# Kernel optimization log

Measured on AMD Instinct MI355X. Metric: run time of the kernel, lower is better.

## Reference

```python
import jax, jax.numpy as jnp
import numpy as np
import math

D_MODEL = 512
DK = D_MODEL // 4      # per-head dim = 128
DH = D_MODEL // 8      # half-head dim = 64
BS, QL, SL = 4, 2048, 2048


def setup_inputs() -> dict:
    key = jax.random.key(0)
    ks = jax.random.split(key, 16)
    h = D_MODEL // 2
    inp = {
        "q": jax.random.normal(ks[0], (2, BS, QL, h), jnp.float32),
        "k": jax.random.normal(ks[1], (2, BS, SL, h), jnp.float32),
        "v": jax.random.normal(ks[2], (2, BS, SL, h), jnp.float32),
        "q_spa_embed": jax.random.normal(ks[3], (BS, 1, DK, DK), jnp.float32) * 0.1,
        "kv_spa_embed": jax.random.normal(ks[4], (BS, SL, DK, DK), jnp.float32) * 0.1,
        "attention_bias": jax.random.normal(ks[5], (BS, SL), jnp.float32),
        "mask": jax.random.randint(ks[6], (BS, SL), 0, 2, jnp.int32),
        # Linear weights stored [in, out] (torch Linear(in,out).weight.T)
        "W_qa": jax.random.normal(ks[7], (h, h // 2), jnp.float32) / math.sqrt(h),
        "W_qb": jax.random.normal(ks[8], (h, h // 2), jnp.float32) / math.sqrt(h),
        "W_ka": jax.random.normal(ks[9], (h, h // 2), jnp.float32) / math.sqrt(h),
        "W_kb": jax.random.normal(ks[10], (h, h // 2), jnp.float32) / math.sqrt(h),
        "W_va": jax.random.normal(ks[11], (h, h // 2), jnp.float32) / math.sqrt(h),
        "W_vb": jax.random.normal(ks[12], (h, h // 2), jnp.float32) / math.sqrt(h),
        "W_oa": jax.random.normal(ks[13], (h, h), jnp.float32) / math.sqrt(h),
        "W_ob": jax.random.normal(ks[14], (h, h), jnp.float32) / math.sqrt(h),
    }
    return inp


def _make_heads(xa, xb):
    # xa, xb: [bs, L, d_model//4] -> [bs, 4, L, dk] with head pattern
    # (a0,b0),(a1,b0),(a0,b1),(a1,b1)
    bs, L, _ = xa.shape
    xa = xa.reshape(bs, L, 2, DH)
    xb = xb.reshape(bs, L, 2, DH)
    xa = jnp.tile(xa, (1, 1, 2, 1))            # [bs,L,4,DH]
    xb = jnp.repeat(xb, 2, axis=2)             # [bs,L,4,DH]
    return jnp.concatenate([xa, xb], axis=-1).transpose(0, 2, 1, 3)  # [bs,4,L,DK]


def reference(q, k, v, q_spa_embed, kv_spa_embed, attention_bias, mask,
              W_qa, W_qb, W_ka, W_kb, W_va, W_vb, W_oa, W_ob):
    bs, ql = q.shape[1], q.shape[2]
    sl = k.shape[2]
    qh = _make_heads(q[0] @ W_qa, q[1] @ W_qb)   # [bs,4,ql,DK]
    kh = _make_heads(k[0] @ W_ka, k[1] @ W_kb)   # [bs,4,sl,DK]
    vh = _make_heads(v[0] @ W_va, v[1] @ W_vb)   # [bs,4,sl,DK]

    # per-token spatial rotation (seq_len == kv_spa_embed.shape[1] branch)
    qh = jnp.einsum('bij,bhqj->bhqi', q_spa_embed[:, 0], qh)
    kh = jnp.einsum('bsij,bhsj->bhsi', kv_spa_embed, kh)

    scores = jnp.einsum('bhqd,bhsd->bhqs', qh, kh) / math.sqrt(D_MODEL // 4)
    scores = scores + mask.astype(scores.dtype)[:, None, None, :] * (-1e9)
    attn = jax.nn.softmax(scores - attention_bias[:, None, None, :], axis=-1)
    # dropout: identity (eval mode)
    out = jnp.einsum('bhqs,bhsd->bhqd', attn, vh)          # [bs,4,ql,DK]

    out = out.reshape(bs, 4, ql, 2, DH)
    oa = out[:, :, :, 0].transpose(0, 2, 1, 3).reshape(bs, ql, -1) @ W_oa
    ob = out[:, :, :, 1].transpose(0, 2, 1, 3).reshape(bs, ql, -1) @ W_ob
    return jnp.stack([oa, ob], axis=0), attn
```

## Files before the change

kernel.cpp:

```cpp
#include <hip/hip_runtime.h>
#include <math.h>

#define QL 2048
#define SL 2048
#define BS 4
#define NH 4
#define FSZ ((size_t)BS * QL * 128)

typedef short bf16x8 __attribute__((ext_vector_type(8)));
typedef float f32x4 __attribute__((ext_vector_type(4)));

__device__ __forceinline__ short to_bf16_rne(float x) {
    unsigned u = __float_as_uint(x);
    unsigned r = u + 0x7fffu + ((u >> 16) & 1u);
    return (short)(r >> 16);
}

__global__ __launch_bounds__(256) void proj_gemm(
    const float* __restrict__ q, const float* __restrict__ k, const float* __restrict__ v,
    const float* __restrict__ Wqa, const float* __restrict__ Wqb,
    const float* __restrict__ Wka, const float* __restrict__ Wkb,
    const float* __restrict__ Wva, const float* __restrict__ Wvb,
    float* __restrict__ ws)
{
    int id = blockIdx.z;
    const float* X; const float* W;
    const size_t HALF = (size_t)BS * QL * 256;
    switch (id) {
      case 0: X = q;        W = Wqa; break;
      case 1: X = q + HALF; W = Wqb; break;
      case 2: X = k;        W = Wka; break;
      case 3: X = k + HALF; W = Wkb; break;
      case 4: X = v;        W = Wva; break;
      default:X = v + HALF; W = Wvb; break;
    }
    float* Y = ws + (size_t)id * FSZ;
    int m0 = blockIdx.x * 64;
    int n0 = blockIdx.y * 64;
    __shared__ float At[64][68];
    __shared__ float Bt[64][68];
    int t = threadIdx.x;
    int tx = t & 15, ty = t >> 4;
    float acc[4][4] = {};
    for (int kc = 0; kc < 256; kc += 64) {
        for (int f = t; f < 1024; f += 256) {
            int row = f >> 4, c4 = (f & 15) * 4;
            *(float4*)&At[row][c4] = *(const float4*)(X + (size_t)(m0 + row) * 256 + kc + c4);
        }
        for (int f = t; f < 1024; f += 256) {
            int row = f >> 4, c4 = (f & 15) * 4;
            *(float4*)&Bt[row][c4] = *(const float4*)(W + (size_t)(kc + row) * 128 + n0 + c4);
        }
        __syncthreads();
        for (int j = 0; j < 64; j += 4) {
            float4 a4[4], b4[4];
            #pragma unroll
            for (int i = 0; i < 4; i++) a4[i] = *(const float4*)&At[ty * 4 + i][j];
            #pragma unroll
            for (int jj = 0; jj < 4; jj++) b4[jj] = *(const float4*)&Bt[j + jj][tx * 4];
            #pragma unroll
            for (int i = 0; i < 4; i++) {
                #pragma unroll
                for (int jj = 0; jj < 4; jj++) {
                    float av = ((const float*)&a4[i])[jj];
                    acc[i][0] += av * b4[jj].x;
                    acc[i][1] += av * b4[jj].y;
                    acc[i][2] += av * b4[jj].z;
                    acc[i][3] += av * b4[jj].w;
                }
            }
        }
        __syncthreads();
    }
    for (int i = 0; i < 4; i++) {
        float4 o = make_float4(acc[i][0], acc[i][1], acc[i][2], acc[i][3]);
        *(float4*)(Y + (size_t)(m0 + ty * 4 + i) * 128 + n0 + tx * 4) = o;
    }
}

__global__ __launch_bounds__(256) void rot_kernel(
    const float* __restrict__ ha, const float* __restrict__ hb,
    const float* __restrict__ E0, int per_token,
    float* __restrict__ outp)
{
    int tkn = blockIdx.x;
    int b = blockIdx.y;
    const float* E = E0 + (per_token ? ((size_t)(b * SL + tkn) * 16384)
                                     : ((size_t)b * 16384));
    __shared__ float hv[4][128];
    __shared__ float outl[4][128];
    int tid = threadIdx.x;
    size_t tok = (size_t)(b * QL + tkn) * 128;
    for (int idx = tid; idx < 512; idx += 256) {
        int h = idx >> 7, d = idx & 127;
        float val = (d < 64) ? ha[tok + (h & 1) * 64 + d]
                             : hb[tok + (h >> 1) * 64 + (d - 64)];
        hv[h][d] = val;
    }
    __syncthreads();
    int w = tid >> 6, lane = tid & 63;
    int half = lane >> 5, l5 = lane & 31;
    for (int it = 0; it < 16; ++it) {
        int i = w * 32 + it * 2 + half;
        float4 e = *(const float4*)(E + (size_t)i * 128 + l5 * 4);
        float acc[4];
        #pragma unroll
        for (int h = 0; h < 4; h++) {
            float4 x = *(const float4*)&hv[h][l5 * 4];
            acc[h] = e.x * x.x + e.y * x.y + e.z * x.z + e.w * x.w;
        }
        #pragma unroll
        for (int off = 1; off < 32; off <<= 1) {
            #pragma unroll
            for (int h = 0; h < 4; h++) acc[h] += __shfl_xor(acc[h], off);
        }
        if (l5 < 4) outl[l5][i] = acc[l5];
    }
    __syncthreads();
    for (int idx = tid; idx < 512; idx += 256) {
        int h = idx >> 7, d = idx & 127;
        outp[((size_t)(b * NH + h) * QL + tkn) * 128 + d] = outl[h][d];
    }
}

__global__ __launch_bounds__(256) void score_mfma_kernel(
    const float* __restrict__ qrot, const float* __restrict__ krot,
    const float* __restrict__ bias, const int* __restrict__ mask,
    float* __restrict__ attn, float* __restrict__ stats)
{
    __shared__ short lA[128 * 64];
    __shared__ short lB[128 * 64];
    __shared__ float redM[128][2];
    __shared__ float redS[128][2];

    int bid = blockIdx.x;
    int wg = (bid & 7) * 512 + (bid >> 3);
    int bh = wg >> 8;
    int qt = (wg >> 4) & 15, st = wg & 15;
    int q0 = qt * 128, s0 = st * 128;
    int b = bh >> 2;

    const float* Ag = qrot + ((size_t)bh * QL + q0) * 128;
    const float* Bg = krot + ((size_t)bh * SL + s0) * 128;

    int t = threadIdx.x;
    int srow = t >> 1, shalf = t & 1;
    int l = t & 63, w = t >> 6;
    int wr = w >> 1, wc = w & 1;
    int lr = l & 15, kb = l >> 4;

    f32x4 acc[4][4] = {};

    for (int kc = 0; kc < 128; kc += 32) {
        {
            const float* srcA = Ag + (size_t)srow * 128 + kc + shalf * 16;
            const float* srcB = Bg + (size_t)srow * 128 + kc + shalf * 16;
            float xa[16], xb[16];
            #pragma unroll
            for (int j = 0; j < 4; j++) {
                *(float4*)&xa[j * 4] = *(const float4*)(srcA + j * 4);
                *(float4*)&xb[j * 4] = *(const float4*)(srcB + j * 4);
            }
            bf16x8 aH0, aL0, aH1, aL1, bH0, bL0, bH1, bL1;
            #pragma unroll
            for (int j = 0; j < 8; j++) {
                short h = to_bf16_rne(xa[j]);
                float hf = __uint_as_float(((unsigned)(unsigned short)h) << 16);
                aH0[j] = h; aL0[j] = to_bf16_rne(xa[j] - hf);
                h = to_bf16_rne(xa[j + 8]);
                hf = __uint_as_float(((unsigned)(unsigned short)h) << 16);
                aH1[j] = h; aL1[j] = to_bf16_rne(xa[j + 8] - hf);
                h = to_bf16_rne(xb[j]);
                hf = __uint_as_float(((unsigned)(unsigned short)h) << 16);
                bH0[j] = h; bL0[j] = to_bf16_rne(xb[j] - hf);
                h = to_bf16_rne(xb[j + 8]);
                hf = __uint_as_float(((unsigned)(unsigned short)h) << 16);
                bH1[j] = h; bL1[j] = to_bf16_rne(xb[j + 8] - hf);
            }
            int base = srow * 64, r7 = srow & 7;
            *(bf16x8*)&lA[base + (((4 * shalf + 0) ^ r7) * 8)] = aH0;
            *(bf16x8*)&lA[base + (((4 * shalf + 1) ^ r7) * 8)] = aL0;
            *(bf16x8*)&lA[base + (((4 * shalf + 2) ^ r7) * 8)] = aH1;
            *(bf16x8*)&lA[base + (((4 * shalf + 3) ^ r7) * 8)] = aL1;
            *(bf16x8*)&lB[base + (((4 * shalf + 0) ^ r7) * 8)] = bH0;
            *(bf16x8*)&lB[base + (((4 * shalf + 1) ^ r7) * 8)] = bL0;
            *(bf16x8*)&lB[base + (((4 * shalf + 2) ^ r7) * 8)] = bH1;
            *(bf16x8*)&lB[base + (((4 * shalf + 3) ^ r7) * 8)] = bL1;
        }
        __syncthreads();

        bf16x8 ah[4], al[4], bhv[4], blv[4];
        #pragma unroll
        for (int m = 0; m < 4; m++) {
            int r = wr * 64 + m * 16 + lr;
            int r7 = r & 7, base = r * 64;
            ah[m] = *(bf16x8*)&lA[base + (((2 * kb + 0) ^ r7) * 8)];
            al[m] = *(bf16x8*)&lA[base + (((2 * kb + 1) ^ r7) * 8)];
        }
        #pragma unroll
        for (int n = 0; n < 4; n++) {
            int r = wc * 64 + n * 16 + lr;
            int r7 = r & 7, base = r * 64;
            bhv[n] = *(bf16x8*)&lB[base + (((2 * kb + 0) ^ r7) * 8)];
            blv[n] = *(bf16x8*)&lB[base + (((2 * kb + 1) ^ r7) * 8)];
        }
        #pragma unroll
        for (int m = 0; m < 4; m++) {
            #pragma unroll
            for (int n = 0; n < 4; n++) {
                acc[m][n] = __builtin_amdgcn_mfma_f32_16x16x32_bf16(ah[m], bhv[n], acc[m][n], 0, 0, 0);
                acc[m][n] = __builtin_amdgcn_mfma_f32_16x16x32_bf16(ah[m], blv[n], acc[m][n], 0, 0, 0);
                acc[m][n] = __builtin_amdgcn_mfma_f32_16x16x32_bf16(al[m], bhv[n], acc[m][n], 0, 0, 0);
            }
        }
        __syncthreads();
    }

    const float scale = 0.08838834764831845f;
    #pragma unroll
    for (int n = 0; n < 4; n++) {
        int gs = s0 + wc * 64 + n * 16 + lr;
        float adj = -1e9f * (float)mask[b * SL + gs] - bias[b * SL + gs];
        #pragma unroll
        for (int m = 0; m < 4; m++) {
            int gq = q0 + wr * 64 + m * 16 + kb * 4;
            float* dst = attn + ((size_t)bh * QL + gq) * SL + gs;
            f32x4 c = acc[m][n];
            c[0] = c[0] * scale + adj;
            c[1] = c[1] * scale + adj;
            c[2] = c[2] * scale + adj;
            c[3] = c[3] * scale + adj;
            acc[m][n] = c;
            dst[0 * SL] = c[0];
            dst[1 * SL] = c[1];
            dst[2 * SL] = c[2];
            dst[3 * SL] = c[3];
        }
    }

    #pragma unroll
    for (int m = 0; m < 4; m++) {
        #pragma unroll
        for (int i = 0; i < 4; i++) {
            float rm = fmaxf(fmaxf(acc[m][0][i], acc[m][1][i]),
                             fmaxf(acc[m][2][i], acc[m][3][i]));
            rm = fmaxf(rm, __shfl_xor(rm, 1));
            rm = fmaxf(rm, __shfl_xor(rm, 2));
            rm = fmaxf(rm, __shfl_xor(rm, 4));
            rm = fmaxf(rm, __shfl_xor(rm, 8));
            if (lr == 0) redM[wr * 64 + m * 16 + kb * 4 + i][wc] = rm;
        }
    }
    __syncthreads();
    #pragma unroll
    for (int m = 0; m < 4; m++) {
        #pragma unroll
        for (int i = 0; i < 4; i++) {
            int row = wr * 64 + m * 16 + kb * 4 + i;
            float mt = fmaxf(redM[row][0], redM[row][1]);
            float es = __expf(acc[m][0][i] - mt) + __expf(acc[m][1][i] - mt)
                     + __expf(acc[m][2][i] - mt) + __expf(acc[m][3][i] - mt);
            es += __shfl_xor(es, 1);
            es += __shfl_xor(es, 2);
            es += __shfl_xor(es, 4);
            es += __shfl_xor(es, 8);
            if (lr == 0) redS[row][wc] = es;
        }
    }
    __syncthreads();
    if (t < 128) {
        float mt = fmaxf(redM[t][0], redM[t][1]);
        float es = redS[t][0] + redS[t][1];
        size_t r = (size_t)bh * QL + q0 + t;
        stats[(r * 16 + st) * 2 + 0] = mt;
        stats[(r * 16 + st) * 2 + 1] = es;
    }
}

__global__ __launch_bounds__(256) void sreduce_kernel(
    const float* __restrict__ stats,
    float* __restrict__ rowm, float* __restrict__ rowinv)
{
    int r = blockIdx.x * 256 + threadIdx.x;
    const float* src = stats + (size_t)r * 32;
    float4 p[8];
    #pragma unroll
    for (int j = 0; j < 8; j++) p[j] = *(const float4*)(src + j * 4);
    float m = -INFINITY;
    #pragma unroll
    for (int j = 0; j < 8; j++) { m = fmaxf(m, p[j].x); m = fmaxf(m, p[j].z); }
    float s = 0.f;
    #pragma unroll
    for (int j = 0; j < 8; j++) {
        s += p[j].y * __expf(p[j].x - m);
        s += p[j].w * __expf(p[j].z - m);
    }
    rowm[r] = m;
    rowinv[r] = 1.0f / s;
}

__global__ __launch_bounds__(256) void vtrans_kernel(
    const float* __restrict__ va, const float* __restrict__ vb,
    short* __restrict__ vT)
{
    int sblk = blockIdx.x;
    int bh = blockIdx.y;
    int b = bh >> 2, h = bh & 3;
    int hao = (h & 1) * 64, hbo = (h >> 1) * 64;
    __shared__ float vt[32][132];
    int t = threadIdx.x;
    for (int f = t; f < 1024; f += 256) {
        int s = f >> 5, c4 = (f & 31) * 4;
        size_t tok = (size_t)(b * SL + sblk * 32 + s) * 128;
        float4 vv = (c4 < 64) ? *(const float4*)(va + tok + hao + c4)
                              : *(const float4*)(vb + tok + hbo + (c4 - 64));
        *(float4*)&vt[s][c4] = vv;
    }
    __syncthreads();
    int d = t >> 1, shalf = t & 1;
    bf16x8 hi[2], lo[2];
    #pragma unroll
    for (int kb2 = 0; kb2 < 2; kb2++) {
        int kb = shalf * 2 + kb2;
        #pragma unroll
        for (int j = 0; j < 8; j++) {
            float x = vt[kb * 8 + j][d];
            short hh = to_bf16_rne(x);
            float hf = __uint_as_float(((unsigned)(unsigned short)hh) << 16);
            hi[kb2][j] = hh;
            lo[kb2][j] = to_bf16_rne(x - hf);
        }
    }
    size_t base = (((size_t)bh * 64 + sblk) * 128 + d) * 64;
    int d7 = d & 7;
    *(bf16x8*)&vT[base + (size_t)(((2 * (shalf * 2 + 0) + 0) ^ d7) * 8)] = hi[0];
    *(bf16x8*)&vT[base + (size_t)(((2 * (shalf * 2 + 0) + 1) ^ d7) * 8)] = lo[0];
    *(bf16x8*)&vT[base + (size_t)(((2 * (shalf * 2 + 1) + 0) ^ d7) * 8)] = hi[1];
    *(bf16x8*)&vT[base + (size_t)(((2 * (shalf * 2 + 1) + 1) ^ d7) * 8)] = lo[1];
}

__global__ __launch_bounds__(256) void pv_fused_kernel(
    float* __restrict__ attn, const short* __restrict__ vT,
    const float* __restrict__ rowm, const float* __restrict__ rowinv,
    float* __restrict__ outh)
{
    __shared__ short lA[128 * 64];
    __shared__ short lB[128 * 64];

    int bid = blockIdx.x;
    int wg = (bid & 7) * 32 + (bid >> 3);
    int bh = wg >> 4, qt = wg & 15;
    int q0 = qt * 128;

    float* Ag = attn + ((size_t)bh * QL + q0) * SL;
    const short* Bg = vT + (size_t)bh * 64 * 8192;

    int t = threadIdx.x;
    int srow = t >> 1, shalf = t & 1;
    int l = t & 63, w = t >> 6;
    int wr = w >> 1, wc = w & 1;
    int lr = l & 15, kb = l >> 4;

    float rm  = rowm[(size_t)bh * QL + q0 + srow];
    float riv = rowinv[(size_t)bh * QL + q0 + srow];

    f32x4 acc[4][4] = {};

    for (int sblk = 0; sblk < 64; sblk++) {
        {
            float* src = Ag + (size_t)srow * SL + sblk * 32 + shalf * 16;
            float x[16];
            #pragma unroll
            for (int j = 0; j < 4; j++)
                *(float4*)&x[j * 4] = *(const float4*)(src + j * 4);
            #pragma unroll
            for (int j = 0; j < 16; j++)
                x[j] = __expf(x[j] - rm) * riv;
            #pragma unroll
            for (int j = 0; j < 4; j++)
                *(float4*)(src + j * 4) = *(float4*)&x[j * 4];
            bf16x8 h0, l0, h1, l1;
            #pragma unroll
            for (int j = 0; j < 8; j++) {
                short hh = to_bf16_rne(x[j]);
                float hf = __uint_as_float(((unsigned)(unsigned short)hh) << 16);
                h0[j] = hh; l0[j] = to_bf16_rne(x[j] - hf);
                hh = to_bf16_rne(x[j + 8]);
                hf = __uint_as_float(((unsigned)(unsigned short)hh) << 16);
                h1[j] = hh; l1[j] = to_bf16_rne(x[j + 8] - hf);
            }
            int base = srow * 64, r7 = srow & 7;
            *(bf16x8*)&lA[base + (((4 * shalf + 0) ^ r7) * 8)] = h0;
            *(bf16x8*)&lA[base + (((4 * shalf + 1) ^ r7) * 8)] = l0;
            *(bf16x8*)&lA[base + (((4 * shalf + 2) ^ r7) * 8)] = h1;
            *(bf16x8*)&lA[base + (((4 * shalf + 3) ^ r7) * 8)] = l1;
        }
        {
            const bf16x8* src = (const bf16x8*)(Bg + (size_t)sblk * 8192) + t * 4;
            bf16x8 v0 = src[0], v1 = src[1], v2 = src[2], v3 = src[3];
            bf16x8* dst = (bf16x8*)lB + t * 4;
            dst[0] = v0; dst[1] = v1; dst[2] = v2; dst[3] = v3;
        }
        __syncthreads();

        bf16x8 ah[4], al[4], bhv[4], blv[4];
        #pragma unroll
        for (int m = 0; m < 4; m++) {
            int r = wr * 64 + m * 16 + lr;
            int r7 = r & 7, base = r * 64;
            ah[m] = *(bf16x8*)&lA[base + (((2 * kb + 0) ^ r7) * 8)];
            al[m] = *(bf16x8*)&lA[base + (((2 * kb + 1) ^ r7) * 8)];
        }
        #pragma unroll
        for (int n = 0; n < 4; n++) {
            int r = wc * 64 + n * 16 + lr;
            int r7 = r & 7, base = r * 64;
            bhv[n] = *(bf16x8*)&lB[base + (((2 * kb + 0) ^ r7) * 8)];
            blv[n] = *(bf16x8*)&lB[base + (((2 * kb + 1) ^ r7) * 8)];
        }
        #pragma unroll
        for (int m = 0; m < 4; m++) {
            #pragma unroll
            for (int n = 0; n < 4; n++) {
                acc[m][n] = __builtin_amdgcn_mfma_f32_16x16x32_bf16(ah[m], bhv[n], acc[m][n], 0, 0, 0);
                acc[m][n] = __builtin_amdgcn_mfma_f32_16x16x32_bf16(ah[m], blv[n], acc[m][n], 0, 0, 0);
                acc[m][n] = __builtin_amdgcn_mfma_f32_16x16x32_bf16(al[m], bhv[n], acc[m][n], 0, 0, 0);
            }
        }
        __syncthreads();
    }

    #pragma unroll
    for (int n = 0; n < 4; n++) {
        int gd = wc * 64 + n * 16 + lr;
        #pragma unroll
        for (int m = 0; m < 4; m++) {
            int gq = q0 + wr * 64 + m * 16 + kb * 4;
            float* dst = outh + ((size_t)bh * QL + gq) * 128 + gd;
            f32x4 c = acc[m][n];
            dst[0 * 128] = c[0];
            dst[1 * 128] = c[1];
            dst[2 * 128] = c[2];
            dst[3 * 128] = c[3];
        }
    }
}

__global__ __launch_bounds__(256) void oproj_kernel(
    const float* __restrict__ outh, const float* __restrict__ Woa, const float* __restrict__ Wob,
    float* __restrict__ outp)
{
    int bid = blockIdx.x;
    int sel = bid >> 9;
    int rem = bid & 511;
    int b = rem >> 7;
    int rem2 = rem & 127;
    int tt = rem2 >> 2, ot = rem2 & 3;
    int t0 = tt * 64, o0 = ot * 64;
    const float* W = sel ? Wob : Woa;
    int doff = sel ? 64 : 0;
    __shared__ float At[64][68];
    __shared__ float Bt[64][68];
    int t = threadIdx.x;
    int tx = t & 15, ty = t >> 4;
    float acc[4][4] = {};
    for (int kc = 0; kc < 256; kc += 64) {
        int h = kc >> 6;
        for (int f = t; f < 1024; f += 256) {
            int row = f >> 4, c4 = (f & 15) * 4;
            *(float4*)&At[row][c4] =
                *(const float4*)(outh + ((size_t)(b * NH + h) * QL + t0 + row) * 128 + doff + c4);
        }
        for (int f = t; f < 1024; f += 256) {
            int row = f >> 4, c4 = (f & 15) * 4;
            *(float4*)&Bt[row][c4] = *(const float4*)(W + (size_t)(kc + row) * 256 + o0 + c4);
        }
        __syncthreads();
        for (int j = 0; j < 64; j += 4) {
            float4 a4[4], b4[4];
            #pragma unroll
            for (int i = 0; i < 4; i++) a4[i] = *(const float4*)&At[ty * 4 + i][j];
            #pragma unroll
            for (int jj = 0; jj < 4; jj++) b4[jj] = *(const float4*)&Bt[j + jj][tx * 4];
            #pragma unroll
            for (int i = 0; i < 4; i++) {
                #pragma unroll
                for (int jj = 0; jj < 4; jj++) {
                    float av = ((const float*)&a4[i])[jj];
                    acc[i][0] += av * b4[jj].x;
                    acc[i][1] += av * b4[jj].y;
                    acc[i][2] += av * b4[jj].z;
                    acc[i][3] += av * b4[jj].w;
                }
            }
        }
        __syncthreads();
    }
    for (int i = 0; i < 4; i++) {
        float4 o = make_float4(acc[i][0], acc[i][1], acc[i][2], acc[i][3]);
        *(float4*)(outp + ((size_t)((sel * BS + b) * QL) + t0 + ty * 4 + i) * 256 + o0 + tx * 4) = o;
    }
}

extern "C" void kernel_launch(void* const* d_in, const int* in_sizes, int n_in,
                              void* d_out, int out_size, void* d_ws, size_t ws_size,
                              hipStream_t stream)
{
    const float* q    = (const float*)d_in[0];
    const float* k    = (const float*)d_in[1];
    const float* v    = (const float*)d_in[2];
    const float* qse  = (const float*)d_in[3];
    const float* kvse = (const float*)d_in[4];
    const float* bias = (const float*)d_in[5];
    const int*   mask = (const int*)d_in[6];
    const float* Wqa  = (const float*)d_in[7];
    const float* Wqb  = (const float*)d_in[8];
    const float* Wka  = (const float*)d_in[9];
    const float* Wkb  = (const float*)d_in[10];
    const float* Wva  = (const float*)d_in[11];
    const float* Wvb  = (const float*)d_in[12];
    const float* Woa  = (const float*)d_in[13];
    const float* Wob  = (const float*)d_in[14];

    float* outp = (float*)d_out;
    float* attn = outp + (size_t)2 * BS * QL * 256;

    float* ws     = (float*)d_ws;
    float* qa     = ws + 0 * FSZ;
    float* qb     = ws + 1 * FSZ;
    float* ka     = ws + 2 * FSZ;
    float* kb     = ws + 3 * FSZ;
    float* va     = ws + 4 * FSZ;
    float* vb     = ws + 5 * FSZ;
    float* qrot   = ws + 6 * FSZ;
    float* krot   = ws + 10 * FSZ;
    float* outh   = ws + 14 * FSZ;
    float* stats  = outh;
    short* vT     = (short*)(ws + 18 * FSZ);
    float* rowm   = ws + 22 * FSZ;
    float* rowinv = ws + 22 * FSZ + 32768;

    proj_gemm<<<dim3(128, 2, 6), 256, 0, stream>>>(q, k, v, Wqa, Wqb, Wka, Wkb, Wva, Wvb, ws);
    vtrans_kernel<<<dim3(64, 16), 256, 0, stream>>>(va, vb, vT);
    rot_kernel<<<dim3(QL, BS), 256, 0, stream>>>(qa, qb, qse, 0, qrot);
    rot_kernel<<<dim3(SL, BS), 256, 0, stream>>>(ka, kb, kvse, 1, krot);
    score_mfma_kernel<<<4096, 256, 0, stream>>>(qrot, krot, bias, mask, attn, stats);
    sreduce_kernel<<<128, 256, 0, stream>>>(stats, rowm, rowinv);
    pv_fused_kernel<<<256, 256, 0, stream>>>(attn, vT, rowm, rowinv, outh);
    oproj_kernel<<<1024, 256, 0, stream>>>(outh, Woa, Wob, outp);
}
```

Measured before the change: 687.7 us.

## Pre-split rotated Q/K into swizzled bf16 hi/lo tiles in rotation kernel

The rotation kernel now converts its output into bf16 hi/lo pairs and writes them in the exact swizzled LDS tile layout used by the score kernel. The score kernel then stages tiles with plain vector copies instead of loading fp32 and converting each tile. Q/K conversion is no longer repeated across the 16 tiles that reuse each Q or K block, and global bytes read per tile stay the same. In exchange the rotation kernel does extra conversion work, and only half its threads do the store.

```diff
diff --git a/kernel.cpp b/kernel.cpp
--- a/kernel.cpp
+++ b/kernel.cpp
@@ -78,10 +78,10 @@
     }
 }
 
-__global__ __launch_bounds__(256) void rot_kernel(
+__global__ __launch_bounds__(256) void rot_split_kernel(
     const float* __restrict__ ha, const float* __restrict__ hb,
     const float* __restrict__ E0, int per_token,
-    float* __restrict__ outp)
+    short* __restrict__ rotS)
 {
     int tkn = blockIdx.x;
     int b = blockIdx.y;
@@ -117,14 +117,35 @@
         if (l5 < 4) outl[l5][i] = acc[l5];
     }
     __syncthreads();
-    for (int idx = tid; idx < 512; idx += 256) {
-        int h = idx >> 7, d = idx & 127;
-        outp[((size_t)(b * NH + h) * QL + tkn) * 128 + d] = outl[h][d];
+    if (tid < 128) {
+        int h    = tid >> 5;
+        int kcid = (tid >> 3) & 3;
+        int s    = tid & 7;
+        int shalf = s >> 2;
+        int isLo  = s & 1;
+        int jbase = ((s >> 1) & 1) * 8;
+        int dbase = kcid * 32 + shalf * 16 + jbase;
+        bf16x8 outv;
+        #pragma unroll
+        for (int j = 0; j < 8; j++) {
+            float x = outl[h][dbase + j];
+            short hh = to_bf16_rne(x);
+            if (isLo) {
+                float hf = __uint_as_float(((unsigned)(unsigned short)hh) << 16);
+                outv[j] = to_bf16_rne(x - hf);
+            } else {
+                outv[j] = hh;
+            }
+        }
+        int bh = b * NH + h;
+        int row = tkn & 127;
+        size_t base = ((((size_t)bh * 16 + (tkn >> 7)) * 4 + kcid) * 128 + row) * 64;
+        *(bf16x8*)&rotS[base + (size_t)((s ^ (row & 7)) * 8)] = outv;
     }
 }
 
 __global__ __launch_bounds__(256) void score_mfma_kernel(
-    const float* __restrict__ qrot, const float* __restrict__ krot,
+    const short* __restrict__ qrotS, const short* __restrict__ krotS,
     const float* __restrict__ bias, const int* __restrict__ mask,
     float* __restrict__ attn, float* __restrict__ stats)
 {
@@ -140,52 +161,26 @@
     int q0 = qt * 128, s0 = st * 128;
     int b = bh >> 2;
 
-    const float* Ag = qrot + ((size_t)bh * QL + q0) * 128;
-    const float* Bg = krot + ((size_t)bh * SL + s0) * 128;
-
     int t = threadIdx.x;
-    int srow = t >> 1, shalf = t & 1;
     int l = t & 63, w = t >> 6;
     int wr = w >> 1, wc = w & 1;
     int lr = l & 15, kb = l >> 4;
 
+    const short* Abase = qrotS + (((size_t)bh * 16 + qt) * 4) * 8192;
+    const short* Bbase = krotS + (((size_t)bh * 16 + st) * 4) * 8192;
+
     f32x4 acc[4][4] = {};
 
-    for (int kc = 0; kc < 128; kc += 32) {
+    for (int kcid = 0; kcid < 4; kcid++) {
         {
-            const float* srcA = Ag + (size_t)srow * 128 + kc + shalf * 16;
-            const float* srcB = Bg + (size_t)srow * 128 + kc + shalf * 16;
-            float xa[16], xb[16];
-            #pragma unroll
-            for (int j = 0; j < 4; j++) {
-                *(float4*)&xa[j * 4] = *(const float4*)(srcA + j * 4);
-                *(float4*)&xb[j * 4] = *(const float4*)(srcB + j * 4);
-            }
-            bf16x8 aH0, aL0, aH1, aL1, bH0, bL0, bH1, bL1;
-            #pragma unroll
-            for (int j = 0; j < 8; j++) {
-                short h = to_bf16_rne(xa[j]);
-                float hf = __uint_as_float(((unsigned)(unsigned short)h) << 16);
-                aH0[j] = h; aL0[j] = to_bf16_rne(xa[j] - hf);
-                h = to_bf16_rne(xa[j + 8]);
-                hf = __uint_as_float(((unsigned)(unsigned short)h) << 16);
-                aH1[j] = h; aL1[j] = to_bf16_rne(xa[j + 8] - hf);
-                h = to_bf16_rne(xb[j]);
-                hf = __uint_as_float(((unsigned)(unsigned short)h) << 16);
-                bH0[j] = h; bL0[j] = to_bf16_rne(xb[j] - hf);
-                h = to_bf16_rne(xb[j + 8]);
-                hf = __uint_as_float(((unsigned)(unsigned short)h) << 16);
-                bH1[j] = h; bL1[j] = to_bf16_rne(xb[j + 8] - hf);
-            }
-            int base = srow * 64, r7 = srow & 7;
-            *(bf16x8*)&lA[base + (((4 * shalf + 0) ^ r7) * 8)] = aH0;
-            *(bf16x8*)&lA[base + (((4 * shalf + 1) ^ r7) * 8)] = aL0;
-            *(bf16x8*)&lA[base + (((4 * shalf + 2) ^ r7) * 8)] = aH1;
-            *(bf16x8*)&lA[base + (((4 * shalf + 3) ^ r7) * 8)] = aL1;
-            *(bf16x8*)&lB[base + (((4 * shalf + 0) ^ r7) * 8)] = bH0;
-            *(bf16x8*)&lB[base + (((4 * shalf + 1) ^ r7) * 8)] = bL0;
-            *(bf16x8*)&lB[base + (((4 * shalf + 2) ^ r7) * 8)] = bH1;
-            *(bf16x8*)&lB[base + (((4 * shalf + 3) ^ r7) * 8)] = bL1;
+            const bf16x8* srcA = (const bf16x8*)(Abase + (size_t)kcid * 8192) + t * 4;
+            const bf16x8* srcB = (const bf16x8*)(Bbase + (size_t)kcid * 8192) + t * 4;
+            bf16x8 a0 = srcA[0], a1 = srcA[1], a2 = srcA[2], a3 = srcA[3];
+            bf16x8 b0 = srcB[0], b1 = srcB[1], b2 = srcB[2], b3 = srcB[3];
+            bf16x8* dA = (bf16x8*)lA + t * 4;
+            bf16x8* dB = (bf16x8*)lB + t * 4;
+            dA[0] = a0; dA[1] = a1; dA[2] = a2; dA[3] = a3;
+            dB[0] = b0; dB[1] = b1; dB[2] = b2; dB[3] = b3;
         }
         __syncthreads();
 
@@ -532,8 +527,8 @@
     float* kb     = ws + 3 * FSZ;
     float* va     = ws + 4 * FSZ;
     float* vb     = ws + 5 * FSZ;
-    float* qrot   = ws + 6 * FSZ;
-    float* krot   = ws + 10 * FSZ;
+    short* qrotS  = (short*)(ws + 6 * FSZ);
+    short* krotS  = (short*)(ws + 10 * FSZ);
     float* outh   = ws + 14 * FSZ;
     float* stats  = outh;
     short* vT     = (short*)(ws + 18 * FSZ);
@@ -542,9 +537,9 @@
 
     proj_gemm<<<dim3(128, 2, 6), 256, 0, stream>>>(q, k, v, Wqa, Wqb, Wka, Wkb, Wva, Wvb, ws);
     vtrans_kernel<<<dim3(64, 16), 256, 0, stream>>>(va, vb, vT);
-    rot_kernel<<<dim3(QL, BS), 256, 0, stream>>>(qa, qb, qse, 0, qrot);
-    rot_kernel<<<dim3(SL, BS), 256, 0, stream>>>(ka, kb, kvse, 1, krot);
-    score_mfma_kernel<<<4096, 256, 0, stream>>>(qrot, krot, bias, mask, attn, stats);
+    rot_split_kernel<<<dim3(QL, BS), 256, 0, stream>>>(qa, qb, qse, 0, qrotS);
+    rot_split_kernel<<<dim3(SL, BS), 256, 0, stream>>>(ka, kb, kvse, 1, krotS);
+    score_mfma_kernel<<<4096, 256, 0, stream>>>(qrotS, krotS, bias, mask, attn, stats);
     sreduce_kernel<<<128, 256, 0, stream>>>(stats, rowm, rowinv);
     pv_fused_kernel<<<256, 256, 0, stream>>>(attn, vT, rowm, rowinv, outh);
     oproj_kernel<<<1024, 256, 0, stream>>>(outh, Woa, Wob, outp);
```

After: 658.7 us. 4.2% less time.
